# Performance work log

Hardware: AMD Instinct MI355X
Metric: run time of the kernel (lower is better)

## Reference

```python
import jax, jax.numpy as jnp
import numpy as np
from jax.ops import segment_sum

N = 50000
E = 1200000
F_IN = 128
HID = 64
N_CLS = 40


def _sage(x, edge_index, edge_weight, W_l, W_r, b):
    # SAGEConv with mean aggregation; messages optionally scaled by edge_weight.
    src, dst = edge_index[0], edge_index[1]
    msg = x[src] * edge_weight[:, None]            # [E, F] gather + scale
    summ = segment_sum(msg, dst, num_segments=N)   # [N, F] scatter-add
    deg = segment_sum(jnp.ones((E,), x.dtype), dst, num_segments=N)
    agg = summ / jnp.maximum(deg, 1.0)[:, None]    # mean over incoming edges
    return agg @ W_l + x @ W_r + b


def setup_inputs() -> dict:
    key = jax.random.key(0)
    ks = jax.random.split(key, 16)
    def glorot(k, shape):
        fan = shape[0] + shape[1]
        return jax.random.normal(k, shape, jnp.float32) * jnp.sqrt(2.0 / fan)
    return {
        "x0": jax.random.normal(ks[0], (N, F_IN), jnp.float32),
        "edge_index": jax.random.randint(ks[1], (2, E), 0, N),
        "edge_weight": jax.random.uniform(ks[2], (E,), jnp.float32),
        "W1l": glorot(ks[3], (F_IN, HID)), "W1r": glorot(ks[4], (F_IN, HID)),
        "b1": jnp.zeros((HID,), jnp.float32),
        "W2l": glorot(ks[5], (HID, HID)), "W2r": glorot(ks[6], (HID, HID)),
        "b2": jnp.zeros((HID,), jnp.float32),
        "W3l": glorot(ks[7], (HID, HID)), "W3r": glorot(ks[8], (HID, HID)),
        "b3": jnp.zeros((HID,), jnp.float32),
        "Wlin": glorot(ks[9], (3 * HID, N_CLS)),
        "blin": jnp.zeros((N_CLS,), jnp.float32),
    }


def reference(x0, edge_index, edge_weight, W1l, W1r, b1, W2l, W2r, b2,
              W3l, W3r, b3, Wlin, blin):
    # dropout in eval mode (identity)
    x1 = jax.nn.relu(_sage(x0, edge_index, edge_weight, W1l, W1r, b1))
    x2 = jax.nn.relu(_sage(x1, edge_index, edge_weight, W2l, W2r, b2))
    x3 = jax.nn.relu(_sage(x2, edge_index, edge_weight, W3l, W3r, b3))
    x = jnp.concatenate([x1, x2, x3], axis=-1)     # [N, 3*HID]
    logits = x @ Wlin + blin                        # [N, N_CLS]
    return jax.nn.log_softmax(logits, axis=-1)
```

## Files before the change

kernel.cpp:

```cpp
#include <hip/hip_runtime.h>
#include <hip/hip_bf16.h>
#include <math.h>

static constexpr int Nn   = 50000;
static constexpr int Ee   = 1200000;
static constexpr int FIN  = 128;
static constexpr int HID  = 64;
static constexpr int NCLS = 40;

static constexpr int NBK    = (Nn + 255) / 256;
static constexpr int CAP    = 7168;
static constexpr int FSLICE = 4096;
static constexpr int FBLK   = (Ee + FSLICE - 1) / FSLICE;

typedef float f32x4  __attribute__((ext_vector_type(4)));
typedef short short8 __attribute__((ext_vector_type(8)));

__device__ inline unsigned short f2b(float f) {
    unsigned int u = __builtin_bit_cast(unsigned int, f);
    return (unsigned short)((u + 0x7FFFu + ((u >> 16) & 1u)) >> 16);
}
__device__ inline float b2f(unsigned short h) {
    return __builtin_bit_cast(float, (unsigned int)h << 16);
}

__global__ __launch_bounds__(256) void init_kernel(int* __restrict__ bcur) {
    int t = threadIdx.x;
    if (t < NBK) bcur[t] = t * CAP;
}

__global__ __launch_bounds__(1024) void bin_fill_kernel(
    const int* __restrict__ src, const int* __restrict__ dst,
    const float* __restrict__ ew, int* __restrict__ bcur,
    int2* __restrict__ edgeT) {
    __shared__ int hist[NBK];
    __shared__ int gbase[NBK];
    const int tid = threadIdx.x;
    for (int i = tid; i < NBK; i += 1024) hist[i] = 0;
    __syncthreads();
    const int e0 = blockIdx.x * FSLICE;
    const int e1 = min(e0 + FSLICE, Ee);
    for (int e = e0 + tid; e < e1; e += 1024)
        atomicAdd(&hist[dst[e] >> 8], 1);
    __syncthreads();
    for (int b = tid; b < NBK; b += 1024) {
        int c = hist[b];
        gbase[b] = c ? atomicAdd(&bcur[b], c) : 0;
        hist[b] = 0;
    }
    __syncthreads();
    for (int e = e0 + tid; e < e1; e += 1024) {
        int d = dst[e];
        int b = d >> 8;
        int r = atomicAdd(&hist[b], 1);
        edgeT[gbase[b] + r] =
            make_int2(src[e] | ((d & 255) << 16), __builtin_bit_cast(int, ew[e]));
    }
}

__global__ __launch_bounds__(512) void sort_kernel(
    const int* __restrict__ bcur, const int2* __restrict__ edgeT,
    unsigned int* __restrict__ edgeA, int* __restrict__ rowbeg,
    int* __restrict__ rowend) {
    __shared__ int hist[256];
    __shared__ int cur[256];
    __shared__ int wsum[4];
    const int t = threadIdx.x, lane = t & 63, wv = t >> 6;
    const int b = blockIdx.x;
    const int beg = b * CAP;
    const int end = bcur[b];

    if (t < 256) hist[t] = 0;
    __syncthreads();
    for (int e = beg + t; e < end; e += 512)
        atomicAdd(&hist[edgeT[e].x >> 16], 1);
    __syncthreads();

    int v = 0, incl = 0;
    if (t < 256) {
        v = hist[t];
        incl = v;
#pragma unroll
        for (int off = 1; off < 64; off <<= 1) {
            int u = __shfl_up(incl, off);
            if (lane >= off) incl += u;
        }
        if (lane == 63) wsum[wv] = incl;
    }
    __syncthreads();
    if (t < 256) {
        int woff = 0;
#pragma unroll
        for (int w = 0; w < 4; ++w) woff += (w < wv) ? wsum[w] : 0;
        const int base = beg + woff + incl - v;
        const int grow = b * 256 + t;
        if (grow < Nn) { rowbeg[grow] = base; rowend[grow] = base + v; }
        cur[t] = base;
    }
    __syncthreads();

    for (int e = beg + t; e < end; e += 512) {
        int2 ed = edgeT[e];
        int ld = ed.x >> 16;
        int p = atomicAdd(&cur[ld], 1);
        unsigned short wb = f2b(__builtin_bit_cast(float, ed.y));
        edgeA[p] = (unsigned int)(ed.x & 0xFFFF) | ((unsigned int)wb << 16);
    }
}

template <int K, typename XT>
__global__ __launch_bounds__(256) void gemmM_kernel(
    const XT* __restrict__ x, const float* __restrict__ Wl,
    const float* __restrict__ Wr, const float* __restrict__ b,
    unsigned short* __restrict__ yl, float* __restrict__ z) {
    constexpr int LDW = K + 8;
    constexpr int NKT = K / 32;
    __shared__ unsigned short wt[128 * LDW];
    __shared__ float b_s[64];

    const int tid  = threadIdx.x;
    const int row0 = blockIdx.x * 64;

    for (int i = tid; i < K * 64; i += 256) {
        int k = i >> 6, c = i & 63;
        wt[c * LDW + k]        = f2b(Wl[i]);
        wt[(64 + c) * LDW + k] = f2b(Wr[i]);
    }
    if (tid < 64) b_s[tid] = b[tid];
    __syncthreads();

    const int wv   = tid >> 6;
    const int lane = tid & 63;
    const int l15  = lane & 15;
    const int quad = lane >> 4;

    const int arow = row0 + wv * 16 + l15;
    const bool rok = arow < Nn;
    short8 a[NKT];
#pragma unroll
    for (int kt = 0; kt < NKT; ++kt) {
        if (rok) {
            if constexpr (sizeof(XT) == 2) {
                a[kt] = *(const short8*)((const unsigned short*)x +
                                         (size_t)arow * K + kt * 32 + quad * 8);
            } else {
                const float* xp = (const float*)x + (size_t)arow * K + kt * 32 + quad * 8;
                float4 p0 = *(const float4*)xp;
                float4 p1 = *(const float4*)(xp + 4);
                short8 af;
                af[0] = (short)f2b(p0.x); af[1] = (short)f2b(p0.y);
                af[2] = (short)f2b(p0.z); af[3] = (short)f2b(p0.w);
                af[4] = (short)f2b(p1.x); af[5] = (short)f2b(p1.y);
                af[6] = (short)f2b(p1.z); af[7] = (short)f2b(p1.w);
                a[kt] = af;
            }
        } else {
            a[kt] = (short8){0, 0, 0, 0, 0, 0, 0, 0};
        }
    }

    f32x4 acc[8];
#pragma unroll
    for (int ct = 0; ct < 8; ++ct) acc[ct] = (f32x4){0.f, 0.f, 0.f, 0.f};

#pragma unroll
    for (int ct = 0; ct < 8; ++ct) {
        const unsigned short* brow = wt + (ct * 16 + l15) * LDW + quad * 8;
#pragma unroll
        for (int kt = 0; kt < NKT; ++kt) {
            short8 bf = *(const short8*)(brow + kt * 32);
            acc[ct] = __builtin_amdgcn_mfma_f32_16x16x32_bf16(a[kt], bf, acc[ct], 0, 0, 0);
        }
    }

#pragma unroll
    for (int ct = 0; ct < 8; ++ct) {
        int col = ct * 16 + l15;
#pragma unroll
        for (int reg = 0; reg < 4; ++reg) {
            int grow = row0 + wv * 16 + quad * 4 + reg;
            if (grow < Nn) {
                if (col < 64) yl[grow * 64 + col] = f2b(acc[ct][reg]);
                else          z[grow * 64 + col - 64] = acc[ct][reg] + b_s[col - 64];
            }
        }
    }
}

__global__ __launch_bounds__(256) void gather_kernel(
    const int* __restrict__ rowbeg, const int* __restrict__ rowend,
    const unsigned int* __restrict__ edgeA, const unsigned short* __restrict__ yl,
    const float* __restrict__ z, unsigned short* __restrict__ xout) {
    int row  = (blockIdx.x * 256 + threadIdx.x) >> 6;
    int lane = threadIdx.x & 63;
    int beg = rowbeg[row], end = rowend[row];
    float acc = 0.f;
    int e = beg;
    for (; e + 8 <= end; e += 8) {
        unsigned int eb[8];
        float vv[8];
#pragma unroll
        for (int j = 0; j < 8; ++j) eb[j] = edgeA[e + j];
#pragma unroll
        for (int j = 0; j < 8; ++j) vv[j] = b2f(yl[(eb[j] & 0xFFFF) * 64 + lane]);
#pragma unroll
        for (int j = 0; j < 8; ++j)
            acc += vv[j] * b2f((unsigned short)(eb[j] >> 16));
    }
    for (; e < end; ++e) {
        unsigned int ee = edgeA[e];
        acc += b2f(yl[(ee & 0xFFFF) * 64 + lane]) * b2f((unsigned short)(ee >> 16));
    }
    float deg = (float)(end - beg);
    float v = acc / fmaxf(deg, 1.f) + z[row * 64 + lane];
    xout[row * 64 + lane] = f2b(fmaxf(v, 0.f));
}

__global__ __launch_bounds__(256) void final_kernel(
    const unsigned short* __restrict__ x1, const unsigned short* __restrict__ x2,
    const unsigned short* __restrict__ x3, const float* __restrict__ Wlin,
    const float* __restrict__ blin, float* __restrict__ out) {
    __shared__ unsigned short wt[48 * 200];

    const int tid  = threadIdx.x;
    const int row0 = blockIdx.x * 64;

    for (int i = tid; i < 48 * 200; i += 256) wt[i] = 0;
    __syncthreads();
    for (int i = tid; i < 192 * 40; i += 256) {
        int k = i / 40, n = i % 40;
        wt[n * 200 + k] = f2b(Wlin[i]);
    }
    __syncthreads();

    const int wv   = tid >> 6;
    const int lane = tid & 63;
    const int l15  = lane & 15;
    const int quad = lane >> 4;

    const int arow = row0 + wv * 16 + l15;
    const bool rok = arow < Nn;
    const unsigned short* xarr[3] = {x1, x2, x3};
    short8 a[6];
#pragma unroll
    for (int ks = 0; ks < 6; ++ks) {
        if (rok)
            a[ks] = *(const short8*)(xarr[ks >> 1] + (size_t)arow * 64 +
                                     (ks & 1) * 32 + quad * 8);
        else
            a[ks] = (short8){0, 0, 0, 0, 0, 0, 0, 0};
    }

    f32x4 acc[3];
#pragma unroll
    for (int nt = 0; nt < 3; ++nt) {
        acc[nt] = (f32x4){0.f, 0.f, 0.f, 0.f};
        const unsigned short* brow = wt + (nt * 16 + l15) * 200 + quad * 8;
#pragma unroll
        for (int ks = 0; ks < 6; ++ks) {
            short8 b = *(const short8*)(brow + ks * 32);
            acc[nt] = __builtin_amdgcn_mfma_f32_16x16x32_bf16(a[ks], b, acc[nt], 0, 0, 0);
        }
    }

    const bool c2ok = l15 < 8;
    const float b0 = blin[l15];
    const float b1 = blin[16 + l15];
    const float b2 = c2ok ? blin[32 + l15] : 0.f;

#pragma unroll
    for (int reg = 0; reg < 4; ++reg) {
        float v0 = acc[0][reg] + b0;
        float v1 = acc[1][reg] + b1;
        float v2 = c2ok ? acc[2][reg] + b2 : -INFINITY;
        float mx = fmaxf(fmaxf(v0, v1), v2);
#pragma unroll
        for (int off = 1; off < 16; off <<= 1) mx = fmaxf(mx, __shfl_xor(mx, off));
        float s = expf(v0 - mx) + expf(v1 - mx) + (c2ok ? expf(v2 - mx) : 0.f);
#pragma unroll
        for (int off = 1; off < 16; off <<= 1) s += __shfl_xor(s, off);
        float lse = mx + logf(s);
        int grow = row0 + wv * 16 + quad * 4 + reg;
        if (grow < Nn) {
            out[grow * NCLS + l15]      = v0 - lse;
            out[grow * NCLS + 16 + l15] = v1 - lse;
            if (c2ok) out[grow * NCLS + 32 + l15] = v2 - lse;
        }
    }
}

extern "C" void kernel_launch(void* const* d_in, const int* in_sizes, int n_in,
                              void* d_out, int out_size, void* d_ws, size_t ws_size,
                              hipStream_t stream) {
    const float* x0  = (const float*)d_in[0];
    const int*   ei  = (const int*)d_in[1];
    const float* ew  = (const float*)d_in[2];
    const float* W1l = (const float*)d_in[3];
    const float* W1r = (const float*)d_in[4];
    const float* b1  = (const float*)d_in[5];
    const float* W2l = (const float*)d_in[6];
    const float* W2r = (const float*)d_in[7];
    const float* b2  = (const float*)d_in[8];
    const float* W3l = (const float*)d_in[9];
    const float* W3r = (const float*)d_in[10];
    const float* b3  = (const float*)d_in[11];
    const float* Wlin = (const float*)d_in[12];
    const float* blin = (const float*)d_in[13];
    float* out = (float*)d_out;

    const int* src = ei;
    const int* dst = ei + Ee;

    const size_t N64 = (size_t)Nn * 64;
    const size_t REG = (size_t)NBK * CAP;
    char* ws = (char*)d_ws;
    int*   bcur   = (int*)ws;
    int*   rowbeg = bcur + 256;
    int*   rowend = rowbeg + 50048;
    int2*  edgeT  = (int2*)(rowend + 50048);
    unsigned int* edgeA = (unsigned int*)(edgeT + REG);
    unsigned short* yl  = (unsigned short*)(edgeA + REG);
    float* zb     = (float*)(yl + N64);
    unsigned short* x1 = (unsigned short*)(zb + N64);
    unsigned short* x2 = x1 + N64;
    unsigned short* x3 = x2 + N64;

    const int gemm_blocks = (Nn + 63) / 64;
    const int row_blocks  = Nn / 4;
    const int fin_blocks  = (Nn + 63) / 64;

    init_kernel<<<1, 256, 0, stream>>>(bcur);
    bin_fill_kernel<<<FBLK, 1024, 0, stream>>>(src, dst, ew, bcur, edgeT);
    sort_kernel<<<NBK, 512, 0, stream>>>(bcur, edgeT, edgeA, rowbeg, rowend);

    gemmM_kernel<FIN, float><<<gemm_blocks, 256, 0, stream>>>(x0, W1l, W1r, b1, yl, zb);
    gather_kernel<<<row_blocks, 256, 0, stream>>>(rowbeg, rowend, edgeA, yl, zb, x1);

    gemmM_kernel<HID, unsigned short><<<gemm_blocks, 256, 0, stream>>>(x1, W2l, W2r, b2, yl, zb);
    gather_kernel<<<row_blocks, 256, 0, stream>>>(rowbeg, rowend, edgeA, yl, zb, x2);

    gemmM_kernel<HID, unsigned short><<<gemm_blocks, 256, 0, stream>>>(x2, W3l, W3r, b3, yl, zb);
    gather_kernel<<<row_blocks, 256, 0, stream>>>(rowbeg, rowend, edgeA, yl, zb, x3);

    final_kernel<<<fin_blocks, 256, 0, stream>>>(x1, x2, x3, Wlin, blin, out);
}
```

Before: 292.6 us.

## Split gathered features into two 32-wide planes and stream halves separately

The gemm now writes the neighbour-projected features into two separate feature planes of 32 bf16 columns each. The gather kernel runs twice as many blocks, one feature half per block. Each wavefront handles two edges at once (32 lanes per edge) and combines them with a cross-lane shuffle. The root-term buffer z shrinks from fp32 to bf16, and edge and z loads and output stores use nontemporal hints. The goal is to shrink each gathered row to 64 bytes so the random gathers have a smaller L2 working set per pass and better locality. The cost is reading the edge list twice, extra shuffle work, and reduced precision in z.

```diff
diff --git a/kernel.cpp b/kernel.cpp
--- a/kernel.cpp
+++ b/kernel.cpp
@@ -12,6 +12,8 @@
 static constexpr int CAP    = 7168;
 static constexpr int FSLICE = 4096;
 static constexpr int FBLK   = (Ee + FSLICE - 1) / FSLICE;
+
+static constexpr int GROWB = 12500;
 
 typedef float f32x4  __attribute__((ext_vector_type(4)));
 typedef short short8 __attribute__((ext_vector_type(8)));
@@ -112,7 +114,7 @@
 __global__ __launch_bounds__(256) void gemmM_kernel(
     const XT* __restrict__ x, const float* __restrict__ Wl,
     const float* __restrict__ Wr, const float* __restrict__ b,
-    unsigned short* __restrict__ yl, float* __restrict__ z) {
+    unsigned short* __restrict__ yl, unsigned short* __restrict__ z) {
     constexpr int LDW = K + 8;
     constexpr int NKT = K / 32;
     __shared__ unsigned short wt[128 * LDW];
@@ -180,8 +182,12 @@
         for (int reg = 0; reg < 4; ++reg) {
             int grow = row0 + wv * 16 + quad * 4 + reg;
             if (grow < Nn) {
-                if (col < 64) yl[grow * 64 + col] = f2b(acc[ct][reg]);
-                else          z[grow * 64 + col - 64] = acc[ct][reg] + b_s[col - 64];
+                if (col < 64) {
+                    int plane = col >> 5, off = col & 31;
+                    yl[(size_t)plane * Nn * 32 + grow * 32 + off] = f2b(acc[ct][reg]);
+                } else {
+                    z[grow * 64 + col - 64] = f2b(acc[ct][reg] + b_s[col - 64]);
+                }
             }
         }
     }
@@ -190,30 +196,45 @@
 __global__ __launch_bounds__(256) void gather_kernel(
     const int* __restrict__ rowbeg, const int* __restrict__ rowend,
     const unsigned int* __restrict__ edgeA, const unsigned short* __restrict__ yl,
-    const float* __restrict__ z, unsigned short* __restrict__ xout) {
-    int row  = (blockIdx.x * 256 + threadIdx.x) >> 6;
-    int lane = threadIdx.x & 63;
+    const unsigned short* __restrict__ z, unsigned short* __restrict__ xout) {
+    const int half = blockIdx.x / GROWB;
+    const int rblk = blockIdx.x % GROWB;
+    const int wv   = threadIdx.x >> 6;
+    const int lane = threadIdx.x & 63;
+    const int row  = rblk * 4 + wv;
+    const int e2   = lane >> 5;
+    const int f    = lane & 31;
+    const unsigned short* ylh = yl + (size_t)half * Nn * 32;
+
     int beg = rowbeg[row], end = rowend[row];
     float acc = 0.f;
     int e = beg;
     for (; e + 8 <= end; e += 8) {
-        unsigned int eb[8];
-        float vv[8];
-#pragma unroll
-        for (int j = 0; j < 8; ++j) eb[j] = edgeA[e + j];
-#pragma unroll
-        for (int j = 0; j < 8; ++j) vv[j] = b2f(yl[(eb[j] & 0xFFFF) * 64 + lane]);
-#pragma unroll
-        for (int j = 0; j < 8; ++j)
+        unsigned int eb[4];
+        float vv[4];
+#pragma unroll
+        for (int j = 0; j < 4; ++j)
+            eb[j] = __builtin_nontemporal_load(&edgeA[e + 2 * j + e2]);
+#pragma unroll
+        for (int j = 0; j < 4; ++j) vv[j] = b2f(ylh[(eb[j] & 0xFFFF) * 32 + f]);
+#pragma unroll
+        for (int j = 0; j < 4; ++j)
             acc += vv[j] * b2f((unsigned short)(eb[j] >> 16));
     }
-    for (; e < end; ++e) {
-        unsigned int ee = edgeA[e];
-        acc += b2f(yl[(ee & 0xFFFF) * 64 + lane]) * b2f((unsigned short)(ee >> 16));
-    }
-    float deg = (float)(end - beg);
-    float v = acc / fmaxf(deg, 1.f) + z[row * 64 + lane];
-    xout[row * 64 + lane] = f2b(fmaxf(v, 0.f));
+    for (; e < end; e += 2) {
+        if (e + e2 < end) {
+            unsigned int ee = __builtin_nontemporal_load(&edgeA[e + e2]);
+            acc += b2f(ylh[(ee & 0xFFFF) * 32 + f]) * b2f((unsigned short)(ee >> 16));
+        }
+    }
+    acc += __shfl_xor(acc, 32);
+    if (lane < 32) {
+        float deg = (float)(end - beg);
+        float v = acc / fmaxf(deg, 1.f) +
+                  b2f(__builtin_nontemporal_load(&z[row * 64 + half * 32 + lane]));
+        __builtin_nontemporal_store(f2b(fmaxf(v, 0.f)),
+                                    &xout[row * 64 + half * 32 + lane]);
+    }
 }
 
 __global__ __launch_bounds__(256) void final_kernel(
@@ -320,13 +341,13 @@
     int2*  edgeT  = (int2*)(rowend + 50048);
     unsigned int* edgeA = (unsigned int*)(edgeT + REG);
     unsigned short* yl  = (unsigned short*)(edgeA + REG);
-    float* zb     = (float*)(yl + N64);
-    unsigned short* x1 = (unsigned short*)(zb + N64);
-    unsigned short* x2 = x1 + N64;
-    unsigned short* x3 = x2 + N64;
+    unsigned short* zb  = yl + N64;
+    unsigned short* x1  = zb + N64;
+    unsigned short* x2  = x1 + N64;
+    unsigned short* x3  = x2 + N64;
 
     const int gemm_blocks = (Nn + 63) / 64;
-    const int row_blocks  = Nn / 4;
+    const int gth_blocks  = 2 * GROWB;
     const int fin_blocks  = (Nn + 63) / 64;
 
     init_kernel<<<1, 256, 0, stream>>>(bcur);
@@ -334,13 +355,13 @@
     sort_kernel<<<NBK, 512, 0, stream>>>(bcur, edgeT, edgeA, rowbeg, rowend);
 
     gemmM_kernel<FIN, float><<<gemm_blocks, 256, 0, stream>>>(x0, W1l, W1r, b1, yl, zb);
-    gather_kernel<<<row_blocks, 256, 0, stream>>>(rowbeg, rowend, edgeA, yl, zb, x1);
+    gather_kernel<<<gth_blocks, 256, 0, stream>>>(rowbeg, rowend, edgeA, yl, zb, x1);
 
     gemmM_kernel<HID, unsigned short><<<gemm_blocks, 256, 0, stream>>>(x1, W2l, W2r, b2, yl, zb);
-    gather_kernel<<<row_blocks, 256, 0, stream>>>(rowbeg, rowend, edgeA, yl, zb, x2);
+    gather_kernel<<<gth_blocks, 256, 0, stream>>>(rowbeg, rowend, edgeA, yl, zb, x2);
 
     gemmM_kernel<HID, unsigned short><<<gemm_blocks, 256, 0, stream>>>(x2, W3l, W3r, b3, yl, zb);
-    gather_kernel<<<row_blocks, 256, 0, stream>>>(rowbeg, rowend, edgeA, yl, zb, x3);
+    gather_kernel<<<gth_blocks, 256, 0, stream>>>(rowbeg, rowend, edgeA, yl, zb, x3);
 
     final_kernel<<<fin_blocks, 256, 0, stream>>>(x1, x2, x3, Wlin, blin, out);
 }
```

Result: slower. 380.5 us (+30.0%).
